# Kernel tuning notes

Hardware: AMD Instinct MI355X
Metric: run time of the kernel (lower is better)

The kernel has to match this reference:

```python
import jax, jax.numpy as jnp
import numpy as np

NUM_ROUTES = 1152
NUM_CAPS = 10
IN_CH = 8
OUT_CH = 16
NUM_ITERS = 3
BATCH = 256


def squash(s, axis=-1, eps=1e-9):
    # standard capsule squash over the capsule-vector (out_channels) axis
    sq_norm = jnp.sum(s * s, axis=axis, keepdims=True)
    return (sq_norm / (1.0 + sq_norm)) * (s / jnp.sqrt(sq_norm + eps))


def setup_inputs() -> dict:
    key = jax.random.key(0)
    kx, kw = jax.random.split(key)
    x = jax.random.normal(kx, (BATCH, NUM_ROUTES, IN_CH), dtype=jnp.float32)
    # kaiming_uniform-ish init: bound = sqrt(6 / fan_in), fan_in = in_channels
    bound = float(np.sqrt(6.0 / IN_CH))
    W = jax.random.uniform(kw, (1, NUM_ROUTES, NUM_CAPS, OUT_CH, IN_CH),
                           dtype=jnp.float32, minval=-bound, maxval=bound)
    return {"x": x, "W": W}


def reference(x, W):
    # x: [B, R, I]; W: [1, R, C, O, I]
    B = x.shape[0]
    Wr = W[0]  # [R, C, O, I]
    # u_hat = W @ x  -> [B, R, C, O] (equivalent to matmul with x unsqueezed)
    u_hat = jnp.einsum('rcoi,bri->brco', Wr, x)

    b_ij = jnp.zeros((NUM_ROUTES, NUM_CAPS), dtype=x.dtype)  # shared over batch
    v_j = None
    c_ij = None
    for it in range(NUM_ITERS):
        c_ij = jax.nn.softmax(b_ij, axis=0)                 # softmax over routes
        s_j = jnp.einsum('rc,brco->bco', c_ij, u_hat)       # [B, C, O]
        v_j = squash(s_j, axis=-1)
        if it < NUM_ITERS - 1:
            # agreement: u_hat^T v, averaged over batch
            a_ij = jnp.einsum('brco,bco->brc', u_hat, v_j)  # [B, R, C]
            b_ij = b_ij + jnp.mean(a_ij, axis=0)

    # match torch output shapes: v_j.squeeze(1) -> [B, C, O, 1]; c_ij -> [B, R, C, 1, 1]
    v_out = v_j[..., None]
    c_out = jnp.broadcast_to(c_ij[None, :, :, None, None],
                             (B, NUM_ROUTES, NUM_CAPS, 1, 1))
    return v_out, c_out
```

## Files before the change

kernel.cpp:

```cpp
#include <hip/hip_runtime.h>
#include <math.h>


typedef __attribute__((ext_vector_type(8))) short short8v;
typedef __attribute__((ext_vector_type(4))) float f32x4;

__device__ __forceinline__ unsigned short f2bf(float f) {
    unsigned u = __float_as_uint(f);
    u += 0x7FFFu + ((u >> 16) & 1u);
    return (unsigned short)(u >> 16);
}
__device__ __forceinline__ float bf2f(unsigned short h) {
    return __uint_as_float(((unsigned)h) << 16);
}

__global__ __launch_bounds__(256) void k_prep(const float* __restrict__ x,
                                              const float* __restrict__ W,
                                              unsigned short* __restrict__ xh,
                                              unsigned short* __restrict__ xl,
                                              unsigned short* __restrict__ wph,
                                              unsigned short* __restrict__ wpl,
                                              unsigned short* __restrict__ xTh,
                                              unsigned short* __restrict__ xTl)
{
    const int tid = threadIdx.x;
    if (blockIdx.x < 2304) {
        const int i = blockIdx.x * 256 + tid;
        const float4 v = reinterpret_cast<const float4*>(x)[i];
        const unsigned short h0 = f2bf(v.x), h1 = f2bf(v.y), h2 = f2bf(v.z), h3 = f2bf(v.w);
        const unsigned short l0 = f2bf(v.x - bf2f(h0)), l1 = f2bf(v.y - bf2f(h1)),
                             l2 = f2bf(v.z - bf2f(h2)), l3 = f2bf(v.w - bf2f(h3));
        reinterpret_cast<uint2*>(xh)[i] =
            make_uint2((unsigned)h0 | ((unsigned)h1 << 16), (unsigned)h2 | ((unsigned)h3 << 16));
        reinterpret_cast<uint2*>(xl)[i] =
            make_uint2((unsigned)l0 | ((unsigned)l1 << 16), (unsigned)l2 | ((unsigned)l3 << 16));
    } else if (blockIdx.x < 2880) {
        __shared__ float raw[2560];
        const int r0 = (blockIdx.x - 2304) * 2;
        const float sc = 1.0f / 1152.0f;
        const float4* __restrict__ W4 = reinterpret_cast<const float4*>(W) + (size_t)r0 * 320;
#pragma unroll
        for (int q = 0; q < 3; ++q) {
            const int idx = q * 256 + tid;
            if (idx < 640) *reinterpret_cast<float4*>(&raw[idx * 4]) = W4[idx];
        }
        __syncthreads();
#pragma unroll
        for (int q = 0; q < 10; ++q) {
            const int idx = q * 256 + tid;
            const int n = idx >> 4, kloc = idx & 15;
            const int rl = kloc >> 3, i = kloc & 7, c = n >> 4, o = n & 15;
            const float wv = raw[rl * 1280 + c * 128 + o * 8 + i] * sc;
            const unsigned short h = f2bf(wv);
            const size_t off = (size_t)n * 9216 + r0 * 8 + kloc;
            wph[off] = h;
            wpl[off] = f2bf(wv - bf2f(h));
        }
    } else {
        __shared__ short Th[16][256];
        __shared__ short Tl[16][256];
        const int m0 = (blockIdx.x - 2880) * 16;
        const int b = tid;
#pragma unroll
        for (int q = 0; q < 4; ++q) {
            const float4 v = reinterpret_cast<const float4*>(x)[(size_t)b * 2304 + (m0 >> 2) + q];
            const unsigned short h0 = f2bf(v.x), h1 = f2bf(v.y), h2 = f2bf(v.z), h3 = f2bf(v.w);
            Th[q * 4 + 0][b] = (short)h0;
            Th[q * 4 + 1][b] = (short)h1;
            Th[q * 4 + 2][b] = (short)h2;
            Th[q * 4 + 3][b] = (short)h3;
            Tl[q * 4 + 0][b] = (short)f2bf(v.x - bf2f(h0));
            Tl[q * 4 + 1][b] = (short)f2bf(v.y - bf2f(h1));
            Tl[q * 4 + 2][b] = (short)f2bf(v.z - bf2f(h2));
            Tl[q * 4 + 3][b] = (short)f2bf(v.w - bf2f(h3));
        }
        __syncthreads();
        const int m = tid >> 4, seg = tid & 15;
        const size_t o = (size_t)(m0 + m) * 256 + seg * 16;
        *reinterpret_cast<uint4*>(xTh + o) = *reinterpret_cast<const uint4*>(&Th[m][seg * 16]);
        *reinterpret_cast<uint4*>(xTh + o + 8) = *reinterpret_cast<const uint4*>(&Th[m][seg * 16 + 8]);
        *reinterpret_cast<uint4*>(xTl + o) = *reinterpret_cast<const uint4*>(&Tl[m][seg * 16]);
        *reinterpret_cast<uint4*>(xTl + o + 8) = *reinterpret_cast<const uint4*>(&Tl[m][seg * 16 + 8]);
    }
}

__global__ __launch_bounds__(256) void k_sM(const unsigned short* __restrict__ xh,
                                            const unsigned short* __restrict__ xl,
                                            const unsigned short* __restrict__ wph,
                                            const unsigned short* __restrict__ wpl,
                                            float* __restrict__ s_part)
{
    __shared__ alignas(16) short Bs[2][12][80][8];
    const int bid  = blockIdx.x;
    const int xcd  = bid & 7;
    const int j    = bid >> 3;
    const int kb   = (j % 12) * 8 + xcd;
    const int mtnt = j / 12;
    const int mt = mtnt >> 1;
    const int nt = mtnt & 1;
    const int tid  = threadIdx.x;
    const int w    = tid >> 6;
    const int lane = tid & 63;
    const int l15  = lane & 15;
    const int lqw  = lane >> 4;
    const int row  = mt * 64 + w * 16 + l15;
    const int n0   = nt * 80;

    short8v ah[3], al[3];
    const size_t arow = (size_t)row * 9216 + kb * 96 + lqw * 8;
#pragma unroll
    for (int ks = 0; ks < 3; ++ks) {
        ah[ks] = *reinterpret_cast<const short8v*>(xh + arow + ks * 32);
        al[ks] = *reinterpret_cast<const short8v*>(xl + arow + ks * 32);
    }

    for (int idx = tid; idx < 960; idx += 256) {
        const int n = idx / 12, ch = idx % 12;
        const size_t g = (size_t)(n0 + n) * 9216 + kb * 96 + ch * 8;
        *reinterpret_cast<short8v*>(&Bs[0][ch][n][0]) =
            *reinterpret_cast<const short8v*>(wph + g);
        *reinterpret_cast<short8v*>(&Bs[1][ch][n][0]) =
            *reinterpret_cast<const short8v*>(wpl + g);
    }
    __syncthreads();

    f32x4 acc[5];
#pragma unroll
    for (int t = 0; t < 5; ++t) acc[t] = (f32x4){0.f, 0.f, 0.f, 0.f};

#pragma unroll
    for (int ks = 0; ks < 3; ++ks) {
        const int ch = ks * 4 + lqw;
#pragma unroll
        for (int t = 0; t < 5; ++t) {
            const short8v bh = *reinterpret_cast<const short8v*>(&Bs[0][ch][t * 16 + l15][0]);
            const short8v bl = *reinterpret_cast<const short8v*>(&Bs[1][ch][t * 16 + l15][0]);
            acc[t] = __builtin_amdgcn_mfma_f32_16x16x32_bf16(ah[ks], bh, acc[t], 0, 0, 0);
            acc[t] = __builtin_amdgcn_mfma_f32_16x16x32_bf16(ah[ks], bl, acc[t], 0, 0, 0);
            acc[t] = __builtin_amdgcn_mfma_f32_16x16x32_bf16(al[ks], bh, acc[t], 0, 0, 0);
        }
    }

    const int crow0 = mt * 64 + w * 16 + lqw * 4;
#pragma unroll
    for (int t = 0; t < 5; ++t) {
#pragma unroll
        for (int v = 0; v < 4; ++v) {
            s_part[((size_t)kb * 256 + crow0 + v) * 160 + n0 + t * 16 + l15] = acc[t][v];
        }
    }
}

__global__ __launch_bounds__(192) void k_rvT(const float* __restrict__ s_part,
                                             unsigned short* __restrict__ vTh,
                                             unsigned short* __restrict__ vTl)
{
    const int b = blockIdx.x;
    const int n = threadIdx.x;
    if (n < 160) {
        const float* p = s_part + (size_t)b * 160 + n;
        float s0 = 0.f, s1 = 0.f, s2 = 0.f, s3 = 0.f, s4 = 0.f, s5 = 0.f, s6 = 0.f, s7 = 0.f;
#pragma unroll
        for (int kbv = 0; kbv < 96; kbv += 8) {
            s0 += p[(size_t)(kbv + 0) * 40960];
            s1 += p[(size_t)(kbv + 1) * 40960];
            s2 += p[(size_t)(kbv + 2) * 40960];
            s3 += p[(size_t)(kbv + 3) * 40960];
            s4 += p[(size_t)(kbv + 4) * 40960];
            s5 += p[(size_t)(kbv + 5) * 40960];
            s6 += p[(size_t)(kbv + 6) * 40960];
            s7 += p[(size_t)(kbv + 7) * 40960];
        }
        const float s = ((s0 + s1) + (s2 + s3)) + ((s4 + s5) + (s6 + s7));
        float sq = s * s;
#pragma unroll
        for (int off = 1; off < 16; off <<= 1) sq += __shfl_xor(sq, off, 16);
        const float scale = (sq / (1.f + sq)) / sqrtf(sq + 1e-9f);
        const float val = s * scale;
        const unsigned short h = f2bf(val);
        vTh[n * 256 + b] = h;
        vTl[n * 256 + b] = f2bf(val - bf2f(h));
    }
}

__global__ __launch_bounds__(128) void k_aM(const unsigned short* __restrict__ vTh,
                                            const unsigned short* __restrict__ vTl,
                                            const unsigned short* __restrict__ xTh,
                                            const unsigned short* __restrict__ xTl,
                                            const float* __restrict__ W,
                                            float* __restrict__ dbp)
{
    __shared__ float dbl[20];
    const int mt = blockIdx.x >> 1;
    const int kh = blockIdx.x & 1;
    const int m0 = mt * 16;
    const int r0 = m0 >> 3;
    const int b0 = kh * 128;
    const int tid  = threadIdx.x;
    const int w    = tid >> 6;
    const int lane = tid & 63;
    const int l15  = lane & 15;
    const int lqw  = lane >> 4;
    if (tid < 20) dbl[tid] = 0.f;

    const size_t xbase = (size_t)(m0 + l15) * 256 + b0 + lqw * 8;

    f32x4 acc[5];
#pragma unroll
    for (int t = 0; t < 5; ++t) acc[t] = (f32x4){0.f, 0.f, 0.f, 0.f};

#pragma unroll
    for (int ks = 0; ks < 4; ++ks) {
        const short8v bh = *reinterpret_cast<const short8v*>(xTh + xbase + ks * 32);
        const short8v bl = *reinterpret_cast<const short8v*>(xTl + xbase + ks * 32);
#pragma unroll
        for (int t = 0; t < 5; ++t) {
            const size_t vbase = (size_t)(w * 80 + t * 16 + l15) * 256 + b0 + lqw * 8 + ks * 32;
            const short8v ah = *reinterpret_cast<const short8v*>(vTh + vbase);
            const short8v al = *reinterpret_cast<const short8v*>(vTl + vbase);
            acc[t] = __builtin_amdgcn_mfma_f32_16x16x32_bf16(ah, bh, acc[t], 0, 0, 0);
            acc[t] = __builtin_amdgcn_mfma_f32_16x16x32_bf16(ah, bl, acc[t], 0, 0, 0);
            acc[t] = __builtin_amdgcn_mfma_f32_16x16x32_bf16(al, bh, acc[t], 0, 0, 0);
        }
    }

    __syncthreads();
    const int rloc = l15 >> 3;
    const int i = l15 & 7;
    const int r = r0 + rloc;
#pragma unroll
    for (int t = 0; t < 5; ++t) {
        const int c = w * 5 + t;
        const float* wp = &W[(((size_t)(r * 10 + c) * 16 + lqw * 4) * 8) + i];
        float pv = wp[0] * acc[t][0] + wp[8] * acc[t][1] + wp[16] * acc[t][2] + wp[24] * acc[t][3];
        pv += __shfl_xor(pv, 16);
        pv += __shfl_xor(pv, 32);
        pv += __shfl_xor(pv, 1);
        pv += __shfl_xor(pv, 2);
        pv += __shfl_xor(pv, 4);
        if ((lane & 55) == 0)
            dbl[rloc * 10 + c] = pv;
    }
    __syncthreads();
    if (tid < 20) dbp[(size_t)kh * 11520 + (r0 + tid / 10) * 10 + (tid % 10)] = dbl[tid];
}

__global__ __launch_bounds__(128) void k_sm(const float* __restrict__ bprev,
                                            const float* __restrict__ dbp,
                                            float* __restrict__ bnew,
                                            float* __restrict__ cij)
{
    __shared__ float red[2];
    __shared__ float red2[2];
    const int c = blockIdx.x;
    const int tid = threadIdx.x;
    float bv[9];
#pragma unroll
    for (int j = 0; j < 9; ++j) {
        const int idx = (tid + j * 128) * 10 + c;
        const float d = dbp[idx] + dbp[11520 + idx];
        bv[j] = (bprev ? bprev[idx] : 0.f) + d * (1.0f / 256.0f);
    }
    float mx = bv[0];
#pragma unroll
    for (int j = 1; j < 9; ++j) mx = fmaxf(mx, bv[j]);
#pragma unroll
    for (int off = 1; off < 64; off <<= 1) mx = fmaxf(mx, __shfl_xor(mx, off, 64));
    if ((tid & 63) == 0) red[tid >> 6] = mx;
    __syncthreads();
    mx = fmaxf(red[0], red[1]);
    float es[9], lsum = 0.f;
#pragma unroll
    for (int j = 0; j < 9; ++j) { es[j] = expf(bv[j] - mx); lsum += es[j]; }
#pragma unroll
    for (int off = 1; off < 64; off <<= 1) lsum += __shfl_xor(lsum, off, 64);
    if ((tid & 63) == 0) red2[tid >> 6] = lsum;
    __syncthreads();
    const float inv = 1.f / (red2[0] + red2[1]);
#pragma unroll
    for (int j = 0; j < 9; ++j) {
        const int idx = (tid + j * 128) * 10 + c;
        bnew[idx] = bv[j];
        cij[idx] = es[j] * inv;
    }
}

__global__ __launch_bounds__(256) void k_scale2(const float* __restrict__ W,
                                                const float* __restrict__ cw,
                                                unsigned short* __restrict__ wph,
                                                unsigned short* __restrict__ wpl)
{
    __shared__ float raw[2560];
    __shared__ float cl[20];
    const int r0 = blockIdx.x * 2;
    const int tid = threadIdx.x;
    if (tid < 20) cl[tid] = cw[r0 * 10 + tid];
    const float4* __restrict__ W4 = reinterpret_cast<const float4*>(W) + (size_t)r0 * 320;
#pragma unroll
    for (int q = 0; q < 3; ++q) {
        const int idx = q * 256 + tid;
        if (idx < 640) *reinterpret_cast<float4*>(&raw[idx * 4]) = W4[idx];
    }
    __syncthreads();
#pragma unroll
    for (int q = 0; q < 10; ++q) {
        const int idx = q * 256 + tid;
        const int n = idx >> 4, kloc = idx & 15;
        const int rl = kloc >> 3, i = kloc & 7, c = n >> 4, o = n & 15;
        const float wv = raw[rl * 1280 + c * 128 + o * 8 + i] * cl[rl * 10 + c];
        const unsigned short h = f2bf(wv);
        const size_t off = (size_t)n * 9216 + r0 * 8 + kloc;
        wph[off] = h;
        wpl[off] = f2bf(wv - bf2f(h));
    }
}

__global__ __launch_bounds__(256) void k_rvc(const float* __restrict__ s_part,
                                             const float* __restrict__ cij,
                                             float* __restrict__ out)
{
    const int tid = threadIdx.x;
    if (blockIdx.x < 160) {
        const int e = blockIdx.x * 256 + tid;
        float s0 = 0.f, s1 = 0.f, s2 = 0.f, s3 = 0.f;
#pragma unroll
        for (int kbv = 0; kbv < 96; kbv += 4) {
            s0 += s_part[(size_t)(kbv + 0) * 40960 + e];
            s1 += s_part[(size_t)(kbv + 1) * 40960 + e];
            s2 += s_part[(size_t)(kbv + 2) * 40960 + e];
            s3 += s_part[(size_t)(kbv + 3) * 40960 + e];
        }
        const float s = (s0 + s1) + (s2 + s3);
        float sq = s * s;
#pragma unroll
        for (int off = 1; off < 16; off <<= 1) sq += __shfl_xor(sq, off, 16);
        const float scale = (sq / (1.f + sq)) / sqrtf(sq + 1e-9f);
        out[e] = s * scale;
    } else {
        const int i = (blockIdx.x - 160) * 256 + tid;
        const float4 v = reinterpret_cast<const float4*>(cij)[i % 2880];
        reinterpret_cast<float4*>(out + 40960)[i] = v;
    }
}

extern "C" void kernel_launch(void* const* d_in, const int* in_sizes, int n_in,
                              void* d_out, int out_size, void* d_ws, size_t ws_size,
                              hipStream_t stream)
{
    const float* x = (const float*)d_in[0];
    const float* W = (const float*)d_in[1];
    float* out = (float*)d_out;

    unsigned short* xh  = (unsigned short*)d_ws;
    unsigned short* xl  = xh + 2359296;
    unsigned short* xTh = xl + 2359296;
    unsigned short* xTl = xTh + 2359296;
    unsigned short* wph = xTl + 2359296;
    unsigned short* wpl = wph + 1474560;
    unsigned short* vTh = wpl + 1474560;
    unsigned short* vTl = vTh + 40960;
    float* s_part = (float*)(vTl + 40960 + 32);
    float* b1   = s_part + 3932160;
    float* b2   = b1 + 11520;
    float* c2   = b2 + 11520;
    float* c3   = c2 + 11520;
    float* dbp0 = c3 + 11520;
    float* dbp1 = dbp0 + 23040;

    k_prep<<<3456, 256, 0, stream>>>(x, W, xh, xl, wph, wpl, xTh, xTl);

    k_sM<<<768, 256, 0, stream>>>(xh, xl, wph, wpl, s_part);
    k_rvT<<<256, 192, 0, stream>>>(s_part, vTh, vTl);
    k_aM<<<1152, 128, 0, stream>>>(vTh, vTl, xTh, xTl, W, dbp0);
    k_sm<<<10, 128, 0, stream>>>(nullptr, dbp0, b1, c2);
    k_scale2<<<576, 256, 0, stream>>>(W, c2, wph, wpl);

    k_sM<<<768, 256, 0, stream>>>(xh, xl, wph, wpl, s_part);
    k_rvT<<<256, 192, 0, stream>>>(s_part, vTh, vTl);
    k_aM<<<1152, 128, 0, stream>>>(vTh, vTl, xTh, xTl, W, dbp1);
    k_sm<<<10, 128, 0, stream>>>(b1, dbp1, b2, c3);
    k_scale2<<<576, 256, 0, stream>>>(W, c3, wph, wpl);

    k_sM<<<768, 256, 0, stream>>>(xh, xl, wph, wpl, s_part);
    k_rvc<<<3040, 256, 0, stream>>>(s_part, c3, out);
}
```

Measured before the change: 122.1 us.

## Fuse W scaling and bf16 split into the s-matmul B-tile load

Removes the separate k_scale2 kernels and the W-prep portion of k_prep. Each k_sM block now reads fp32 W directly, scales it by the per-route coupling coefficients, and splits it into bf16 hi/lo pieces while filling shared memory. This drops two launches and the round trip through the wph/wpl workspace. In exchange, each W element is re-read and re-converted by every m-tile block, which adds fp32 global traffic and conversion ALU work to the matmul kernel.

```diff
diff --git a/kernel.cpp b/kernel.cpp
--- a/kernel.cpp
+++ b/kernel.cpp
@@ -15,11 +15,8 @@
 }
 
 __global__ __launch_bounds__(256) void k_prep(const float* __restrict__ x,
-                                              const float* __restrict__ W,
                                               unsigned short* __restrict__ xh,
                                               unsigned short* __restrict__ xl,
-                                              unsigned short* __restrict__ wph,
-                                              unsigned short* __restrict__ wpl,
                                               unsigned short* __restrict__ xTh,
                                               unsigned short* __restrict__ xTl)
 {
@@ -34,32 +31,10 @@
             make_uint2((unsigned)h0 | ((unsigned)h1 << 16), (unsigned)h2 | ((unsigned)h3 << 16));
         reinterpret_cast<uint2*>(xl)[i] =
             make_uint2((unsigned)l0 | ((unsigned)l1 << 16), (unsigned)l2 | ((unsigned)l3 << 16));
-    } else if (blockIdx.x < 2880) {
-        __shared__ float raw[2560];
-        const int r0 = (blockIdx.x - 2304) * 2;
-        const float sc = 1.0f / 1152.0f;
-        const float4* __restrict__ W4 = reinterpret_cast<const float4*>(W) + (size_t)r0 * 320;
-#pragma unroll
-        for (int q = 0; q < 3; ++q) {
-            const int idx = q * 256 + tid;
-            if (idx < 640) *reinterpret_cast<float4*>(&raw[idx * 4]) = W4[idx];
-        }
-        __syncthreads();
-#pragma unroll
-        for (int q = 0; q < 10; ++q) {
-            const int idx = q * 256 + tid;
-            const int n = idx >> 4, kloc = idx & 15;
-            const int rl = kloc >> 3, i = kloc & 7, c = n >> 4, o = n & 15;
-            const float wv = raw[rl * 1280 + c * 128 + o * 8 + i] * sc;
-            const unsigned short h = f2bf(wv);
-            const size_t off = (size_t)n * 9216 + r0 * 8 + kloc;
-            wph[off] = h;
-            wpl[off] = f2bf(wv - bf2f(h));
-        }
     } else {
         __shared__ short Th[16][256];
         __shared__ short Tl[16][256];
-        const int m0 = (blockIdx.x - 2880) * 16;
+        const int m0 = (blockIdx.x - 2304) * 16;
         const int b = tid;
 #pragma unroll
         for (int q = 0; q < 4; ++q) {
@@ -86,11 +61,12 @@
 
 __global__ __launch_bounds__(256) void k_sM(const unsigned short* __restrict__ xh,
                                             const unsigned short* __restrict__ xl,
-                                            const unsigned short* __restrict__ wph,
-                                            const unsigned short* __restrict__ wpl,
+                                            const float* __restrict__ W,
+                                            const float* __restrict__ cw,
                                             float* __restrict__ s_part)
 {
     __shared__ alignas(16) short Bs[2][12][80][8];
+    __shared__ float cl[120];
     const int bid  = blockIdx.x;
     const int xcd  = bid & 7;
     const int j    = bid >> 3;
@@ -105,6 +81,7 @@
     const int lqw  = lane >> 4;
     const int row  = mt * 64 + w * 16 + l15;
     const int n0   = nt * 80;
+    const int r_base = kb * 12;
 
     short8v ah[3], al[3];
     const size_t arow = (size_t)row * 9216 + kb * 96 + lqw * 8;
@@ -114,13 +91,28 @@
         al[ks] = *reinterpret_cast<const short8v*>(xl + arow + ks * 32);
     }
 
+    if (tid < 120) cl[tid] = cw ? cw[r_base * 10 + tid] : (1.0f / 1152.0f);
+    __syncthreads();
+
     for (int idx = tid; idx < 960; idx += 256) {
         const int n = idx / 12, ch = idx % 12;
-        const size_t g = (size_t)(n0 + n) * 9216 + kb * 96 + ch * 8;
-        *reinterpret_cast<short8v*>(&Bs[0][ch][n][0]) =
-            *reinterpret_cast<const short8v*>(wph + g);
-        *reinterpret_cast<short8v*>(&Bs[1][ch][n][0]) =
-            *reinterpret_cast<const short8v*>(wpl + g);
+        const int gn = n0 + n;
+        const int c = gn >> 4, o = gn & 15;
+        const float sc = cl[ch * 10 + c];
+        const float* wp = &W[(size_t)(r_base + ch) * 1280 + c * 128 + o * 8];
+        const float4 w0 = *reinterpret_cast<const float4*>(wp);
+        const float4 w1 = *reinterpret_cast<const float4*>(wp + 4);
+        float v[8] = { w0.x * sc, w0.y * sc, w0.z * sc, w0.w * sc,
+                       w1.x * sc, w1.y * sc, w1.z * sc, w1.w * sc };
+        short8v hv, lv;
+#pragma unroll
+        for (int q = 0; q < 8; ++q) {
+            const unsigned short h = f2bf(v[q]);
+            hv[q] = (short)h;
+            lv[q] = (short)f2bf(v[q] - bf2f(h));
+        }
+        *reinterpret_cast<short8v*>(&Bs[0][ch][n][0]) = hv;
+        *reinterpret_cast<short8v*>(&Bs[1][ch][n][0]) = lv;
     }
     __syncthreads();
 
@@ -285,36 +277,6 @@
     }
 }
 
-__global__ __launch_bounds__(256) void k_scale2(const float* __restrict__ W,
-                                                const float* __restrict__ cw,
-                                                unsigned short* __restrict__ wph,
-                                                unsigned short* __restrict__ wpl)
-{
-    __shared__ float raw[2560];
-    __shared__ float cl[20];
-    const int r0 = blockIdx.x * 2;
-    const int tid = threadIdx.x;
-    if (tid < 20) cl[tid] = cw[r0 * 10 + tid];
-    const float4* __restrict__ W4 = reinterpret_cast<const float4*>(W) + (size_t)r0 * 320;
-#pragma unroll
-    for (int q = 0; q < 3; ++q) {
-        const int idx = q * 256 + tid;
-        if (idx < 640) *reinterpret_cast<float4*>(&raw[idx * 4]) = W4[idx];
-    }
-    __syncthreads();
-#pragma unroll
-    for (int q = 0; q < 10; ++q) {
-        const int idx = q * 256 + tid;
-        const int n = idx >> 4, kloc = idx & 15;
-        const int rl = kloc >> 3, i = kloc & 7, c = n >> 4, o = n & 15;
-        const float wv = raw[rl * 1280 + c * 128 + o * 8 + i] * cl[rl * 10 + c];
-        const unsigned short h = f2bf(wv);
-        const size_t off = (size_t)n * 9216 + r0 * 8 + kloc;
-        wph[off] = h;
-        wpl[off] = f2bf(wv - bf2f(h));
-    }
-}
-
 __global__ __launch_bounds__(256) void k_rvc(const float* __restrict__ s_part,
                                              const float* __restrict__ cij,
                                              float* __restrict__ out)
@@ -355,9 +317,7 @@
     unsigned short* xl  = xh + 2359296;
     unsigned short* xTh = xl + 2359296;
     unsigned short* xTl = xTh + 2359296;
-    unsigned short* wph = xTl + 2359296;
-    unsigned short* wpl = wph + 1474560;
-    unsigned short* vTh = wpl + 1474560;
+    unsigned short* vTh = xTl + 2359296;
     unsigned short* vTl = vTh + 40960;
     float* s_part = (float*)(vTl + 40960 + 32);
     float* b1   = s_part + 3932160;
@@ -367,20 +327,18 @@
     float* dbp0 = c3 + 11520;
     float* dbp1 = dbp0 + 23040;
 
-    k_prep<<<3456, 256, 0, stream>>>(x, W, xh, xl, wph, wpl, xTh, xTl);
-
-    k_sM<<<768, 256, 0, stream>>>(xh, xl, wph, wpl, s_part);
+    k_prep<<<2880, 256, 0, stream>>>(x, xh, xl, xTh, xTl);
+
+    k_sM<<<768, 256, 0, stream>>>(xh, xl, W, nullptr, s_part);
     k_rvT<<<256, 192, 0, stream>>>(s_part, vTh, vTl);
     k_aM<<<1152, 128, 0, stream>>>(vTh, vTl, xTh, xTl, W, dbp0);
     k_sm<<<10, 128, 0, stream>>>(nullptr, dbp0, b1, c2);
-    k_scale2<<<576, 256, 0, stream>>>(W, c2, wph, wpl);
-
-    k_sM<<<768, 256, 0, stream>>>(xh, xl, wph, wpl, s_part);
+
+    k_sM<<<768, 256, 0, stream>>>(xh, xl, W, c2, s_part);
     k_rvT<<<256, 192, 0, stream>>>(s_part, vTh, vTl);
     k_aM<<<1152, 128, 0, stream>>>(vTh, vTl, xTh, xTl, W, dbp1);
     k_sm<<<10, 128, 0, stream>>>(b1, dbp1, b2, c3);
-    k_scale2<<<576, 256, 0, stream>>>(W, c3, wph, wpl);
-
-    k_sM<<<768, 256, 0, stream>>>(xh, xl, wph, wpl, s_part);
+
+    k_sM<<<768, 256, 0, stream>>>(xh, xl, W, c3, s_part);
     k_rvc<<<3040, 256, 0, stream>>>(s_part, c3, out);
 }
```

Result: faster. 111.9 us (-8.4%).
